# Optimization experiments

Measured on AMD Instinct MI355X. Metric: run time of the kernel, lower is better.

## Reference

```python
import math
import jax, jax.numpy as jnp
import numpy as np


def log1mexp(x):
    # Numerically accurate log(1 - exp(x)) for x < 0 (Maechler 2012).
    mask = x > -math.log(2.0)
    return jnp.where(mask, jnp.log(-jnp.expm1(x)), jnp.log1p(-jnp.exp(x)))


def encode_input(pos):
    # pos: [n_vars, batch] log-probs. Output: [2*n_vars+2, batch]
    # row 0 = -inf (false), row 1 = 0 (true), then interleaved pos/neg.
    neg = log1mexp(pos)
    n, b = pos.shape
    inter = jnp.stack([pos, neg], axis=1).reshape(2 * n, b)  # pos at even, neg at odd
    head = jnp.stack([jnp.full((b,), -jnp.inf, pos.dtype), jnp.zeros((b,), pos.dtype)])
    return jnp.concatenate([head, inter], axis=0)


def setup_inputs() -> dict:
    key = jax.random.key(0)
    k0, k1, k2, k3, k4 = jax.random.split(key, 5)
    N_VARS, BATCH = 1024, 4096
    u = jax.random.uniform(k0, (N_VARS, BATCH), minval=1e-6, maxval=1.0 - 1e-6)
    pos = jnp.log(u)  # valid log-probabilities, strictly < 0
    idx0 = jax.random.randint(k1, (8192, 4), 1, 2 * N_VARS + 2)  # product over encoded leaves (skip -inf row)
    idx1 = jax.random.randint(k2, (4096, 8), 0, 8192)            # sum over products
    idx2 = jax.random.randint(k3, (8192, 4), 0, 4096)            # product
    idx3 = jax.random.randint(k4, (2048, 8), 0, 8192)            # sum
    return {"pos": pos, "idx0": idx0, "idx1": idx1, "idx2": idx2, "idx3": idx3}


def reference(pos, idx0, idx1, idx2, idx3):
    x = encode_input(pos)                          # [2050, B]
    x = x[idx0].sum(axis=1)                        # ProductLayer: gather + sum -> [8192, B]
    x = jax.nn.logsumexp(x[idx1], axis=1)          # SumLayer: gather + logsumexp -> [4096, B]
    x = x[idx2].sum(axis=1)                        # ProductLayer -> [8192, B]
    x = jax.nn.logsumexp(x[idx3], axis=1)          # SumLayer -> [2048, B]
    return x
```

## Files before the change

kernel.cpp:

```cpp
#include <hip/hip_runtime.h>
#include <math.h>

#define BATCH   4096
#define NVARS   1024
#define ROWS_P0 8192
#define ROWS_S1 4096
#define ROWS_P2 8192
#define ROWS_S3 2048
#define ENCROWS 2050

#define LOG2E 1.4426950408889634f
#define LN2   0.6931471805599453f

typedef _Float16 h4 __attribute__((ext_vector_type(4)));
typedef float    f2 __attribute__((ext_vector_type(2)));

union HU { h4 h; uint2 u; };

__device__ __forceinline__ float fexp2(float x) { return __builtin_amdgcn_exp2f(x); }
__device__ __forceinline__ float flog2(float x) { return __builtin_amdgcn_logf(x); }

__device__ __forceinline__ float log1mexp_log2(float x) {
    float v = -x;
    float p = 1.0f + v * (-0.5f + v * (0.166666667f + v * (-0.0416666667f + v * 0.00833333333f)));
    float bs = v * p;
    float bd = 1.0f - fexp2(x * LOG2E);
    float arg = (x > -0.6931471805599453f) ? bs : bd;
    return flog2(arg);
}

__device__ __forceinline__ unsigned pk_bf16(float x, float y) {
    unsigned xb = __float_as_uint(x) + 0x8000u;
    unsigned yb = __float_as_uint(y) + 0x8000u;
    return (xb >> 16) | (yb & 0xFFFF0000u);
}
__device__ __forceinline__ float bf_lo(unsigned v) { return __uint_as_float(v << 16); }
__device__ __forceinline__ float bf_hi(unsigned v) { return __uint_as_float(v & 0xFFFF0000u); }
__device__ __forceinline__ f2 mk2(float a, float b) { f2 r; r.x = a; r.y = b; return r; }

__global__ __launch_bounds__(1024, 8) void pipeline_kernel(const float* __restrict__ pos,
                                                           const int4* __restrict__ idx0,
                                                           const int4* __restrict__ idx1,
                                                           const int4* __restrict__ idx2,
                                                           const int4* __restrict__ idx3,
                                                           float* __restrict__ out) {
    __shared__ __align__(16) char pool[65536];
    h4*    enc = reinterpret_cast<h4*>(pool);
    uint2* p0  = reinterpret_cast<uint2*>(pool);
    h4*    s1  = reinterpret_cast<h4*>(pool);
    uint2* p2  = reinterpret_cast<uint2*>(pool);

    const int tid = threadIdx.x;
    const int bid = blockIdx.x;
    const int swz = ((bid & 7) << 7) | (bid >> 3);
    const int c0 = swz * 4;

    {
        const float4 a = *reinterpret_cast<const float4*>(pos + (size_t)tid * BATCH + c0);
        HU ep, en;
        ep.h.x = (_Float16)(a.x * LOG2E); ep.h.y = (_Float16)(a.y * LOG2E);
        ep.h.z = (_Float16)(a.z * LOG2E); ep.h.w = (_Float16)(a.w * LOG2E);
        en.h.x = (_Float16)log1mexp_log2(a.x); en.h.y = (_Float16)log1mexp_log2(a.y);
        en.h.z = (_Float16)log1mexp_log2(a.z); en.h.w = (_Float16)log1mexp_log2(a.w);
        uint2* encu = reinterpret_cast<uint2*>(pool);
        encu[2 + 2 * tid] = ep.u;
        encu[3 + 2 * tid] = en.u;
        if (tid == 0) {
            HU ni, z;
            ni.h.x = ni.h.y = ni.h.z = ni.h.w = (_Float16)(-INFINITY);
            z.h.x = z.h.y = z.h.z = z.h.w = (_Float16)0.f;
            encu[0] = ni.u;
            encu[1] = z.u;
        }
    }
    __syncthreads();

    uint2 hold0[8];
#pragma unroll
    for (int i = 0; i < ROWS_P0 / 1024; ++i) {
        int r = tid + i * 1024;
        int4 ix = idx0[r];
        h4 v0 = enc[ix.x], v1 = enc[ix.y], v2 = enc[ix.z], v3 = enc[ix.w];
        h4 s = (v0 + v1) + (v2 + v3);
        hold0[i] = make_uint2(pk_bf16(fexp2((float)s.x), fexp2((float)s.y)),
                              pk_bf16(fexp2((float)s.z), fexp2((float)s.w)));
    }
    __syncthreads();
#pragma unroll
    for (int i = 0; i < ROWS_P0 / 1024; ++i) p0[tid + i * 1024] = hold0[i];
    __syncthreads();

    h4 hold1[4];
#pragma unroll
    for (int i = 0; i < ROWS_S1 / 1024; ++i) {
        int r = tid + i * 1024;
        int4 a = idx1[2 * r], b = idx1[2 * r + 1];
        uint2 u0 = p0[a.x], u1 = p0[a.y], u2 = p0[a.z], u3 = p0[a.w];
        uint2 u4 = p0[b.x], u5 = p0[b.y], u6 = p0[b.z], u7 = p0[b.w];
        f2 ab = (mk2(bf_lo(u0.x), bf_hi(u0.x)) + mk2(bf_lo(u1.x), bf_hi(u1.x))) +
                (mk2(bf_lo(u2.x), bf_hi(u2.x)) + mk2(bf_lo(u3.x), bf_hi(u3.x)));
        ab = ab + ((mk2(bf_lo(u4.x), bf_hi(u4.x)) + mk2(bf_lo(u5.x), bf_hi(u5.x))) +
                   (mk2(bf_lo(u6.x), bf_hi(u6.x)) + mk2(bf_lo(u7.x), bf_hi(u7.x))));
        f2 cd = (mk2(bf_lo(u0.y), bf_hi(u0.y)) + mk2(bf_lo(u1.y), bf_hi(u1.y))) +
                (mk2(bf_lo(u2.y), bf_hi(u2.y)) + mk2(bf_lo(u3.y), bf_hi(u3.y)));
        cd = cd + ((mk2(bf_lo(u4.y), bf_hi(u4.y)) + mk2(bf_lo(u5.y), bf_hi(u5.y))) +
                   (mk2(bf_lo(u6.y), bf_hi(u6.y)) + mk2(bf_lo(u7.y), bf_hi(u7.y))));
        ab = __builtin_elementwise_max(ab, mk2(1e-37f, 1e-37f));
        cd = __builtin_elementwise_max(cd, mk2(1e-37f, 1e-37f));
        h4 o;
        o.x = (_Float16)flog2(ab.x);
        o.y = (_Float16)flog2(ab.y);
        o.z = (_Float16)flog2(cd.x);
        o.w = (_Float16)flog2(cd.y);
        hold1[i] = o;
    }
    __syncthreads();
#pragma unroll
    for (int i = 0; i < ROWS_S1 / 1024; ++i) s1[tid + i * 1024] = hold1[i];
    __syncthreads();

    uint2 hold2[8];
#pragma unroll
    for (int i = 0; i < ROWS_P2 / 1024; ++i) {
        int r = tid + i * 1024;
        int4 ix = idx2[r];
        h4 v0 = s1[ix.x], v1 = s1[ix.y], v2 = s1[ix.z], v3 = s1[ix.w];
        h4 s = (v0 + v1) + (v2 + v3);
        hold2[i] = make_uint2(pk_bf16(fexp2((float)s.x), fexp2((float)s.y)),
                              pk_bf16(fexp2((float)s.z), fexp2((float)s.w)));
    }
    __syncthreads();
#pragma unroll
    for (int i = 0; i < ROWS_P2 / 1024; ++i) p2[tid + i * 1024] = hold2[i];
    __syncthreads();

#pragma unroll
    for (int i = 0; i < ROWS_S3 / 1024; ++i) {
        int r = tid + i * 1024;
        int4 a = idx3[2 * r], b = idx3[2 * r + 1];
        uint2 u0 = p2[a.x], u1 = p2[a.y], u2 = p2[a.z], u3 = p2[a.w];
        uint2 u4 = p2[b.x], u5 = p2[b.y], u6 = p2[b.z], u7 = p2[b.w];
        f2 ab = (mk2(bf_lo(u0.x), bf_hi(u0.x)) + mk2(bf_lo(u1.x), bf_hi(u1.x))) +
                (mk2(bf_lo(u2.x), bf_hi(u2.x)) + mk2(bf_lo(u3.x), bf_hi(u3.x)));
        ab = ab + ((mk2(bf_lo(u4.x), bf_hi(u4.x)) + mk2(bf_lo(u5.x), bf_hi(u5.x))) +
                   (mk2(bf_lo(u6.x), bf_hi(u6.x)) + mk2(bf_lo(u7.x), bf_hi(u7.x))));
        f2 cd = (mk2(bf_lo(u0.y), bf_hi(u0.y)) + mk2(bf_lo(u1.y), bf_hi(u1.y))) +
                (mk2(bf_lo(u2.y), bf_hi(u2.y)) + mk2(bf_lo(u3.y), bf_hi(u3.y)));
        cd = cd + ((mk2(bf_lo(u4.y), bf_hi(u4.y)) + mk2(bf_lo(u5.y), bf_hi(u5.y))) +
                   (mk2(bf_lo(u6.y), bf_hi(u6.y)) + mk2(bf_lo(u7.y), bf_hi(u7.y))));
        ab = __builtin_elementwise_max(ab, mk2(1e-37f, 1e-37f));
        cd = __builtin_elementwise_max(cd, mk2(1e-37f, 1e-37f));
        float4 o4;
        o4.x = flog2(ab.x) * LN2;
        o4.y = flog2(ab.y) * LN2;
        o4.z = flog2(cd.x) * LN2;
        o4.w = flog2(cd.y) * LN2;
        reinterpret_cast<float4*>(out)[(size_t)r * (BATCH / 4) + swz] = o4;
    }
}

extern "C" void kernel_launch(void* const* d_in, const int* in_sizes, int n_in,
                              void* d_out, int out_size, void* d_ws, size_t ws_size,
                              hipStream_t stream) {
    const float* pos  = (const float*)d_in[0];
    const int4*  idx0 = (const int4*)d_in[1];
    const int4*  idx1 = (const int4*)d_in[2];
    const int4*  idx2 = (const int4*)d_in[3];
    const int4*  idx3 = (const int4*)d_in[4];
    float*       out  = (float*)d_out;
    (void)d_ws; (void)ws_size;

    pipeline_kernel<<<dim3(BATCH / 4), dim3(1024), 0, stream>>>(pos, idx0, idx1, idx2, idx3, out);
}
```

Before: 46.11 us.

## Halve batch columns per block to 2 with 512 threads and 32KB LDS

Each block now handles 2 batch columns instead of 4, with 512 threads and a 32KB shared pool, and launches twice as many blocks. Intermediate values become packed pairs (one 32-bit word per row) instead of 64-bit quads. The aim is to allow more resident blocks per CU through lower LDS use, improving latency hiding for the gather-heavy LDS stages. In exchange, index arrays are re-read by twice as many blocks, each gather moves half the data, and global writes are 8-byte rather than 16-byte.

```diff
diff --git a/kernel.cpp b/kernel.cpp
--- a/kernel.cpp
+++ b/kernel.cpp
@@ -7,15 +7,15 @@
 #define ROWS_S1 4096
 #define ROWS_P2 8192
 #define ROWS_S3 2048
-#define ENCROWS 2050
 
 #define LOG2E 1.4426950408889634f
 #define LN2   0.6931471805599453f
+#define NT    512
 
-typedef _Float16 h4 __attribute__((ext_vector_type(4)));
+typedef _Float16 h2 __attribute__((ext_vector_type(2)));
 typedef float    f2 __attribute__((ext_vector_type(2)));
 
-union HU { h4 h; uint2 u; };
+union H2U { h2 h; unsigned u; };
 
 __device__ __forceinline__ float fexp2(float x) { return __builtin_amdgcn_exp2f(x); }
 __device__ __forceinline__ float flog2(float x) { return __builtin_amdgcn_logf(x); }
@@ -38,124 +38,105 @@
 __device__ __forceinline__ float bf_hi(unsigned v) { return __uint_as_float(v & 0xFFFF0000u); }
 __device__ __forceinline__ f2 mk2(float a, float b) { f2 r; r.x = a; r.y = b; return r; }
 
-__global__ __launch_bounds__(1024, 8) void pipeline_kernel(const float* __restrict__ pos,
-                                                           const int4* __restrict__ idx0,
-                                                           const int4* __restrict__ idx1,
-                                                           const int4* __restrict__ idx2,
-                                                           const int4* __restrict__ idx3,
-                                                           float* __restrict__ out) {
-    __shared__ __align__(16) char pool[65536];
-    h4*    enc = reinterpret_cast<h4*>(pool);
-    uint2* p0  = reinterpret_cast<uint2*>(pool);
-    h4*    s1  = reinterpret_cast<h4*>(pool);
-    uint2* p2  = reinterpret_cast<uint2*>(pool);
+__global__ __launch_bounds__(NT, 8) void pipeline_kernel(const float* __restrict__ pos,
+                                                         const int4* __restrict__ idx0,
+                                                         const int4* __restrict__ idx1,
+                                                         const int4* __restrict__ idx2,
+                                                         const int4* __restrict__ idx3,
+                                                         float* __restrict__ out) {
+    __shared__ __align__(16) char pool[32768];
+    unsigned* pu = reinterpret_cast<unsigned*>(pool);
+    h2*       ph = reinterpret_cast<h2*>(pool);
 
     const int tid = threadIdx.x;
     const int bid = blockIdx.x;
-    const int swz = ((bid & 7) << 7) | (bid >> 3);
-    const int c0 = swz * 4;
+    const int swz = ((bid & 7) << 8) | (bid >> 3);
+    const int c0 = swz * 2;
 
     {
-        const float4 a = *reinterpret_cast<const float4*>(pos + (size_t)tid * BATCH + c0);
-        HU ep, en;
-        ep.h.x = (_Float16)(a.x * LOG2E); ep.h.y = (_Float16)(a.y * LOG2E);
-        ep.h.z = (_Float16)(a.z * LOG2E); ep.h.w = (_Float16)(a.w * LOG2E);
-        en.h.x = (_Float16)log1mexp_log2(a.x); en.h.y = (_Float16)log1mexp_log2(a.y);
-        en.h.z = (_Float16)log1mexp_log2(a.z); en.h.w = (_Float16)log1mexp_log2(a.w);
-        uint2* encu = reinterpret_cast<uint2*>(pool);
-        encu[2 + 2 * tid] = ep.u;
-        encu[3 + 2 * tid] = en.u;
+        float2 A = *reinterpret_cast<const float2*>(pos + (size_t)tid * BATCH + c0);
+        float2 B = *reinterpret_cast<const float2*>(pos + (size_t)(tid + NT) * BATCH + c0);
+        H2U pA, nA, pB, nB;
+        pA.h.x = (_Float16)(A.x * LOG2E);        pA.h.y = (_Float16)(A.y * LOG2E);
+        nA.h.x = (_Float16)log1mexp_log2(A.x);   nA.h.y = (_Float16)log1mexp_log2(A.y);
+        pB.h.x = (_Float16)(B.x * LOG2E);        pB.h.y = (_Float16)(B.y * LOG2E);
+        nB.h.x = (_Float16)log1mexp_log2(B.x);   nB.h.y = (_Float16)log1mexp_log2(B.y);
+        pu[2 + 2 * tid] = pA.u;
+        pu[3 + 2 * tid] = nA.u;
+        pu[2 + 2 * (tid + NT)] = pB.u;
+        pu[3 + 2 * (tid + NT)] = nB.u;
         if (tid == 0) {
-            HU ni, z;
-            ni.h.x = ni.h.y = ni.h.z = ni.h.w = (_Float16)(-INFINITY);
-            z.h.x = z.h.y = z.h.z = z.h.w = (_Float16)0.f;
-            encu[0] = ni.u;
-            encu[1] = z.u;
+            pu[0] = 0xFC00FC00u;
+            pu[1] = 0u;
         }
     }
     __syncthreads();
 
-    uint2 hold0[8];
+    unsigned hold0[16];
 #pragma unroll
-    for (int i = 0; i < ROWS_P0 / 1024; ++i) {
-        int r = tid + i * 1024;
+    for (int i = 0; i < ROWS_P0 / NT; ++i) {
+        int r = tid + i * NT;
         int4 ix = idx0[r];
-        h4 v0 = enc[ix.x], v1 = enc[ix.y], v2 = enc[ix.z], v3 = enc[ix.w];
-        h4 s = (v0 + v1) + (v2 + v3);
-        hold0[i] = make_uint2(pk_bf16(fexp2((float)s.x), fexp2((float)s.y)),
-                              pk_bf16(fexp2((float)s.z), fexp2((float)s.w)));
+        h2 v0 = ph[ix.x], v1 = ph[ix.y], v2 = ph[ix.z], v3 = ph[ix.w];
+        h2 s = (v0 + v1) + (v2 + v3);
+        hold0[i] = pk_bf16(fexp2((float)s.x), fexp2((float)s.y));
     }
     __syncthreads();
 #pragma unroll
-    for (int i = 0; i < ROWS_P0 / 1024; ++i) p0[tid + i * 1024] = hold0[i];
+    for (int i = 0; i < ROWS_P0 / NT; ++i) pu[tid + i * NT] = hold0[i];
     __syncthreads();
 
-    h4 hold1[4];
+    unsigned hold1[8];
 #pragma unroll
-    for (int i = 0; i < ROWS_S1 / 1024; ++i) {
-        int r = tid + i * 1024;
+    for (int i = 0; i < ROWS_S1 / NT; ++i) {
+        int r = tid + i * NT;
         int4 a = idx1[2 * r], b = idx1[2 * r + 1];
-        uint2 u0 = p0[a.x], u1 = p0[a.y], u2 = p0[a.z], u3 = p0[a.w];
-        uint2 u4 = p0[b.x], u5 = p0[b.y], u6 = p0[b.z], u7 = p0[b.w];
-        f2 ab = (mk2(bf_lo(u0.x), bf_hi(u0.x)) + mk2(bf_lo(u1.x), bf_hi(u1.x))) +
-                (mk2(bf_lo(u2.x), bf_hi(u2.x)) + mk2(bf_lo(u3.x), bf_hi(u3.x)));
-        ab = ab + ((mk2(bf_lo(u4.x), bf_hi(u4.x)) + mk2(bf_lo(u5.x), bf_hi(u5.x))) +
-                   (mk2(bf_lo(u6.x), bf_hi(u6.x)) + mk2(bf_lo(u7.x), bf_hi(u7.x))));
-        f2 cd = (mk2(bf_lo(u0.y), bf_hi(u0.y)) + mk2(bf_lo(u1.y), bf_hi(u1.y))) +
-                (mk2(bf_lo(u2.y), bf_hi(u2.y)) + mk2(bf_lo(u3.y), bf_hi(u3.y)));
-        cd = cd + ((mk2(bf_lo(u4.y), bf_hi(u4.y)) + mk2(bf_lo(u5.y), bf_hi(u5.y))) +
-                   (mk2(bf_lo(u6.y), bf_hi(u6.y)) + mk2(bf_lo(u7.y), bf_hi(u7.y))));
+        unsigned u0 = pu[a.x], u1 = pu[a.y], u2 = pu[a.z], u3 = pu[a.w];
+        unsigned u4 = pu[b.x], u5 = pu[b.y], u6 = pu[b.z], u7 = pu[b.w];
+        f2 ab = ((mk2(bf_lo(u0), bf_hi(u0)) + mk2(bf_lo(u1), bf_hi(u1))) +
+                 (mk2(bf_lo(u2), bf_hi(u2)) + mk2(bf_lo(u3), bf_hi(u3)))) +
+                ((mk2(bf_lo(u4), bf_hi(u4)) + mk2(bf_lo(u5), bf_hi(u5))) +
+                 (mk2(bf_lo(u6), bf_hi(u6)) + mk2(bf_lo(u7), bf_hi(u7))));
         ab = __builtin_elementwise_max(ab, mk2(1e-37f, 1e-37f));
-        cd = __builtin_elementwise_max(cd, mk2(1e-37f, 1e-37f));
-        h4 o;
-        o.x = (_Float16)flog2(ab.x);
-        o.y = (_Float16)flog2(ab.y);
-        o.z = (_Float16)flog2(cd.x);
-        o.w = (_Float16)flog2(cd.y);
-        hold1[i] = o;
+        H2U o;
+        o.h.x = (_Float16)flog2(ab.x);
+        o.h.y = (_Float16)flog2(ab.y);
+        hold1[i] = o.u;
     }
     __syncthreads();
 #pragma unroll
-    for (int i = 0; i < ROWS_S1 / 1024; ++i) s1[tid + i * 1024] = hold1[i];
+    for (int i = 0; i < ROWS_S1 / NT; ++i) pu[tid + i * NT] = hold1[i];
     __syncthreads();
 
-    uint2 hold2[8];
+    unsigned hold2[16];
 #pragma unroll
-    for (int i = 0; i < ROWS_P2 / 1024; ++i) {
-        int r = tid + i * 1024;
+    for (int i = 0; i < ROWS_P2 / NT; ++i) {
+        int r = tid + i * NT;
         int4 ix = idx2[r];
-        h4 v0 = s1[ix.x], v1 = s1[ix.y], v2 = s1[ix.z], v3 = s1[ix.w];
-        h4 s = (v0 + v1) + (v2 + v3);
-        hold2[i] = make_uint2(pk_bf16(fexp2((float)s.x), fexp2((float)s.y)),
-                              pk_bf16(fexp2((float)s.z), fexp2((float)s.w)));
+        h2 v0 = ph[ix.x], v1 = ph[ix.y], v2 = ph[ix.z], v3 = ph[ix.w];
+        h2 s = (v0 + v1) + (v2 + v3);
+        hold2[i] = pk_bf16(fexp2((float)s.x), fexp2((float)s.y));
     }
     __syncthreads();
 #pragma unroll
-    for (int i = 0; i < ROWS_P2 / 1024; ++i) p2[tid + i * 1024] = hold2[i];
+    for (int i = 0; i < ROWS_P2 / NT; ++i) pu[tid + i * NT] = hold2[i];
     __syncthreads();
 
 #pragma unroll
-    for (int i = 0; i < ROWS_S3 / 1024; ++i) {
-        int r = tid + i * 1024;
+    for (int i = 0; i < ROWS_S3 / NT; ++i) {
+        int r = tid + i * NT;
         int4 a = idx3[2 * r], b = idx3[2 * r + 1];
-        uint2 u0 = p2[a.x], u1 = p2[a.y], u2 = p2[a.z], u3 = p2[a.w];
-        uint2 u4 = p2[b.x], u5 = p2[b.y], u6 = p2[b.z], u7 = p2[b.w];
-        f2 ab = (mk2(bf_lo(u0.x), bf_hi(u0.x)) + mk2(bf_lo(u1.x), bf_hi(u1.x))) +
-                (mk2(bf_lo(u2.x), bf_hi(u2.x)) + mk2(bf_lo(u3.x), bf_hi(u3.x)));
-        ab = ab + ((mk2(bf_lo(u4.x), bf_hi(u4.x)) + mk2(bf_lo(u5.x), bf_hi(u5.x))) +
-                   (mk2(bf_lo(u6.x), bf_hi(u6.x)) + mk2(bf_lo(u7.x), bf_hi(u7.x))));
-        f2 cd = (mk2(bf_lo(u0.y), bf_hi(u0.y)) + mk2(bf_lo(u1.y), bf_hi(u1.y))) +
-                (mk2(bf_lo(u2.y), bf_hi(u2.y)) + mk2(bf_lo(u3.y), bf_hi(u3.y)));
-        cd = cd + ((mk2(bf_lo(u4.y), bf_hi(u4.y)) + mk2(bf_lo(u5.y), bf_hi(u5.y))) +
-                   (mk2(bf_lo(u6.y), bf_hi(u6.y)) + mk2(bf_lo(u7.y), bf_hi(u7.y))));
+        unsigned u0 = pu[a.x], u1 = pu[a.y], u2 = pu[a.z], u3 = pu[a.w];
+        unsigned u4 = pu[b.x], u5 = pu[b.y], u6 = pu[b.z], u7 = pu[b.w];
+        f2 ab = ((mk2(bf_lo(u0), bf_hi(u0)) + mk2(bf_lo(u1), bf_hi(u1))) +
+                 (mk2(bf_lo(u2), bf_hi(u2)) + mk2(bf_lo(u3), bf_hi(u3)))) +
+                ((mk2(bf_lo(u4), bf_hi(u4)) + mk2(bf_lo(u5), bf_hi(u5))) +
+                 (mk2(bf_lo(u6), bf_hi(u6)) + mk2(bf_lo(u7), bf_hi(u7))));
         ab = __builtin_elementwise_max(ab, mk2(1e-37f, 1e-37f));
-        cd = __builtin_elementwise_max(cd, mk2(1e-37f, 1e-37f));
-        float4 o4;
-        o4.x = flog2(ab.x) * LN2;
-        o4.y = flog2(ab.y) * LN2;
-        o4.z = flog2(cd.x) * LN2;
-        o4.w = flog2(cd.y) * LN2;
-        reinterpret_cast<float4*>(out)[(size_t)r * (BATCH / 4) + swz] = o4;
+        float2 o;
+        o.x = flog2(ab.x) * LN2;
+        o.y = flog2(ab.y) * LN2;
+        *reinterpret_cast<float2*>(out + (size_t)r * BATCH + c0) = o;
     }
 }
 
@@ -170,5 +151,5 @@
     float*       out  = (float*)d_out;
     (void)d_ws; (void)ws_size;
 
-    pipeline_kernel<<<dim3(BATCH / 4), dim3(1024), 0, stream>>>(pos, idx0, idx1, idx2, idx3, out);
+    pipeline_kernel<<<dim3(BATCH / 2), dim3(NT), 0, stream>>>(pos, idx0, idx1, idx2, idx3, out);
 }
```

Measured after the change: 65.88 us. 42.9% more time.
